# Performance work log

Hardware: AMD Instinct MI355X
Metric: run time of the kernel (lower is better)

## Reference

```python
import jax, jax.numpy as jnp
import numpy as np

B, D = 8192, 512
MARGIN, CR_BETA, NUM_CLASSES = 0.2, 0.1, 1000


def setup_inputs() -> dict:
    key = jax.random.key(0)
    k1, k2, k3, k4 = jax.random.split(key, 4)
    return {
        "img": jax.random.normal(k1, (B, D), jnp.float32),
        "txt": jax.random.normal(k2, (B, D), jnp.float32),
        "txt_cr": jax.random.normal(k3, (B, D), jnp.float32),
        "labels": jax.random.randint(k4, (B,), 0, NUM_CLASSES),
        "auto_margin_flag": 1,
        "margin": jnp.full((B,), MARGIN, jnp.float32),  # opt.margin repeated per row
        "cr_beta": CR_BETA,
    }


def _similarity(a, b):
    # row-normalize then full cosine-similarity matrix + matched (diagonal) sims
    an = a / (jnp.linalg.norm(a, axis=1, keepdims=True) + 1e-8)
    bn = b / (jnp.linalg.norm(b, axis=1, keepdims=True) + 1e-8)
    return an @ bn.T, jnp.sum(an * bn, axis=1)


def _dir_loss(sim, labels, margin, auto_flag):
    # semi-hard negative mining per anchor row, fully vectorized.
    # Deterministic stand-in for np.random.choice: first valid negative index.
    diag = jnp.diagonal(sim)                               # sim[idx, idx]
    neg_mask = labels[None, :] != labels[:, None]          # [B,B] negatives
    loss_mat = sim - diag[:, None] + margin[:, None]       # triplet margin term
    valid = neg_mask & (loss_mat > 0) & (loss_mat < margin[:, None])
    valid = jax.lax.stop_gradient(valid)                   # mining is detached (numpy in torch)
    has_valid = jnp.any(valid, axis=1)
    if auto_flag:
        row_ok = (margin >= 0.16) & has_valid
    else:
        row_ok = has_valid
    neg_idx = jnp.argmax(valid, axis=1)                    # first valid negative
    sim_an = jnp.take_along_axis(sim, neg_idx[:, None], axis=1)[:, 0]
    per_row = jax.nn.relu(margin - diag + sim_an)
    return jnp.sum(jnp.where(row_ok, per_row, 0.0))


def _cr_loss(img, txt, txt_cr, labels, auto_flag, margin, cr_beta):
    sim, sm = _similarity(img, txt)
    sim_cr, sm_cr = _similarity(img, txt_cr)
    if auto_flag:
        lam = jnp.abs(jax.lax.stop_gradient(sm_cr)) / jnp.abs(jax.lax.stop_gradient(sm))
        lam = jnp.minimum(lam, 1.0)                        # clamp lambda_cr to <= 1
        margin_cr = (lam + 1.0) * margin / 2.0
    else:
        margin_cr = margin / 2.0
    margin_cr = jax.lax.stop_gradient(margin_cr)
    base = _dir_loss(sim, labels, margin, auto_flag) + _dir_loss(sim.T, labels, margin, auto_flag)
    cr = _dir_loss(sim_cr, labels, margin_cr, auto_flag) + _dir_loss(sim_cr.T, labels, margin_cr, auto_flag)
    return base + cr_beta * cr


def reference(img, txt, txt_cr, labels, auto_margin_flag, margin, cr_beta):
    return _cr_loss(img, txt, txt_cr, labels, bool(auto_margin_flag), margin, cr_beta)
```

## Files before the change

kernel.cpp:

```cpp
#include <hip/hip_runtime.h>
#include <climits>

#define NB 8192
#define ND 512
#define NSPLIT 32
#define RSTART 64
#define RSPAN ((NB - RSTART + NSPLIT - 1) / NSPLIT)


__global__ __launch_bounds__(256) void stats_k(
        const float* __restrict__ img, const float* __restrict__ txt,
        const float* __restrict__ cr, const float* __restrict__ margin,
        const int* __restrict__ flagp,
        float* rnImg, float* rnTxt, float* rnCr,
        float* dgSim, float* dgCr, float* mgCr,
        int* negIdx, int* stragCnt, float* out) {
    int tid = threadIdx.x, bid = blockIdx.x;
    int g = bid * 256 + tid;
    if (g < 4 * NB) negIdx[g] = INT_MAX;
    if (bid == 0 && tid < 8) stragCnt[tid] = 0;
    if (bid == 0 && tid == 0) out[0] = 0.0f;

    int r = bid * 16 + (tid >> 4);
    int q = tid & 15;
    const float4* iv = (const float4*)(img + (size_t)r * ND);
    const float4* tv = (const float4*)(txt + (size_t)r * ND);
    const float4* cv = (const float4*)(cr  + (size_t)r * ND);
    float sii = 0, stt = 0, scc = 0, sit = 0, sic = 0;
    #pragma unroll
    for (int i = 0; i < 8; ++i) {
        int k = q + i * 16;
        float4 x = iv[k], y = tv[k], w = cv[k];
        sii += x.x*x.x + x.y*x.y + x.z*x.z + x.w*x.w;
        stt += y.x*y.x + y.y*y.y + y.z*y.z + y.w*y.w;
        scc += w.x*w.x + w.y*w.y + w.z*w.z + w.w*w.w;
        sit += x.x*y.x + x.y*y.y + x.z*y.z + x.w*y.w;
        sic += x.x*w.x + x.y*w.y + x.z*w.z + x.w*w.w;
    }
    #pragma unroll
    for (int off = 1; off < 16; off <<= 1) {
        sii += __shfl_xor(sii, off); stt += __shfl_xor(stt, off);
        scc += __shfl_xor(scc, off); sit += __shfl_xor(sit, off);
        sic += __shfl_xor(sic, off);
    }
    if (q == 0) {
        float rnI = 1.0f / (sqrtf(sii) + 1e-8f);
        float rnT = 1.0f / (sqrtf(stt) + 1e-8f);
        float rnC = 1.0f / (sqrtf(scc) + 1e-8f);
        float ds = sit * rnI * rnT;
        float dc = sic * rnI * rnC;
        float m  = margin[r];
        float mcr = flagp[0] ? (fminf(fabsf(dc) / fabsf(ds), 1.0f) + 1.0f) * m * 0.5f
                             : m * 0.5f;
        rnImg[r] = rnI; rnTxt[r] = rnT; rnCr[r] = rnC;
        dgSim[r] = ds;  dgCr[r]  = dc;  mgCr[r] = mcr;
    }
}

__device__ inline void pass_arrays(int z,
        const float* img, const float* txt, const float* cr,
        const float* rnImg, const float* rnTxt, const float* rnCr,
        const float* dgSim, const float* dgCr,
        const float* margin, const float* mgCr,
        const float*& A, const float*& B, const float*& rnA, const float*& rnB,
        const float*& dgA, const float*& mgA) {
    if (z == 0)      { A = img; B = txt; rnA = rnImg; rnB = rnTxt; dgA = dgSim; mgA = margin; }
    else if (z == 1) { A = txt; B = img; rnA = rnTxt; rnB = rnImg; dgA = dgSim; mgA = margin; }
    else if (z == 2) { A = img; B = cr;  rnA = rnImg; rnB = rnCr;  dgA = dgCr;  mgA = mgCr;   }
    else             { A = cr;  B = img; rnA = rnCr;  rnB = rnImg; dgA = dgCr;  mgA = mgCr;   }
}

__global__ __launch_bounds__(256) void band_k(
        const float* __restrict__ img, const float* __restrict__ txt,
        const float* __restrict__ cr, const int* __restrict__ labels,
        const int* __restrict__ flagp, const float* __restrict__ margin,
        const float* __restrict__ betap,
        const float* rnImg, const float* rnTxt, const float* rnCr,
        const float* dgSim, const float* dgCr, const float* mgCr,
        int* stragCnt, int* stragList, float* out) {
    __shared__ __align__(16) float As[16][64];
    __shared__ __align__(16) float Bs[16][64];
    __shared__ float aRn[64], aDg[64], aMg[64], colRn[64];
    __shared__ int   aLab[64], colLab[64], resIdx[64];
    __shared__ float blockAcc;

    const int tid = threadIdx.x, z = blockIdx.y, a0 = blockIdx.x * 64;
    const int flag = flagp[0];
    const float *A, *B, *rnA, *rnB, *dgA, *mgA;
    pass_arrays(z, img, txt, cr, rnImg, rnTxt, rnCr, dgSim, dgCr, margin, mgCr,
                A, B, rnA, rnB, dgA, mgA);

    if (tid < 64) {
        int a = a0 + tid;
        float mg = mgA[a];
        aRn[tid] = rnA[a]; aDg[tid] = dgA[a]; aMg[tid] = mg;
        aLab[tid] = labels[a];
        colRn[tid] = rnB[tid]; colLab[tid] = labels[tid];
        resIdx[tid] = (flag && mg < 0.16f) ? -1 : INT_MAX;
    }
    if (tid == 0) blockAcc = 0.0f;

    const int ty4  = (tid >> 4) * 4, tx4 = (tid & 15) * 4;
    const int lrow = tid >> 2,  lk4 = (tid & 3) * 4;

    float acc[4][4];
    #pragma unroll
    for (int i = 0; i < 4; ++i)
        #pragma unroll
        for (int j = 0; j < 4; ++j) acc[i][j] = 0.0f;

    float4 va = *(const float4*)(A + (size_t)(a0 + lrow) * ND + lk4);
    float4 vb = *(const float4*)(B + (size_t)lrow * ND + lk4);
    for (int kc = 0; kc < ND; kc += 16) {
        __syncthreads();
        As[lk4 + 0][lrow] = va.x; As[lk4 + 1][lrow] = va.y;
        As[lk4 + 2][lrow] = va.z; As[lk4 + 3][lrow] = va.w;
        Bs[lk4 + 0][lrow] = vb.x; Bs[lk4 + 1][lrow] = vb.y;
        Bs[lk4 + 2][lrow] = vb.z; Bs[lk4 + 3][lrow] = vb.w;
        if (kc + 16 < ND) {
            va = *(const float4*)(A + (size_t)(a0 + lrow) * ND + kc + 16 + lk4);
            vb = *(const float4*)(B + (size_t)lrow * ND + kc + 16 + lk4);
        }
        __syncthreads();
        #pragma unroll
        for (int k = 0; k < 16; ++k) {
            float4 av = *(const float4*)&As[k][ty4];
            float4 bv = *(const float4*)&Bs[k][tx4];
            float ar[4] = {av.x, av.y, av.z, av.w};
            float br[4] = {bv.x, bv.y, bv.z, bv.w};
            #pragma unroll
            for (int i = 0; i < 4; ++i)
                #pragma unroll
                for (int j = 0; j < 4; ++j)
                    acc[i][j] = fmaf(ar[i], br[j], acc[i][j]);
        }
    }
    __syncthreads();

    #pragma unroll
    for (int i = 0; i < 4; ++i) {
        int r = ty4 + i;
        float mgv = aMg[r];
        if (flag && mgv < 0.16f) continue;
        float dg = aDg[r], rna = aRn[r];
        int la = aLab[r];
        #pragma unroll
        for (int j = 0; j < 4; ++j) {
            int c = tx4 + j;
            if (colLab[c] == la) continue;
            float v  = acc[i][j] * rna * colRn[c];
            float lm = v - dg + mgv;
            if (lm > 0.0f && lm < mgv) atomicMin(&resIdx[r], c);
        }
    }
    __syncthreads();

    #pragma unroll
    for (int i = 0; i < 4; ++i) {
        int r = ty4 + i;
        int w = resIdx[r];
        if (w < 0 || w == INT_MAX) continue;
        int c = w - tx4;
        if (c < 0 || c > 3) continue;
        float v  = acc[i][c] * aRn[r] * colRn[w];
        float lm = v - aDg[r] + aMg[r];
        atomicAdd(&blockAcc, lm);
    }
    __syncthreads();

    if (tid < 64 && resIdx[tid] == INT_MAX) {
        int pos = atomicAdd(&stragCnt[z], 1);
        stragList[z * NB + pos] = a0 + tid;
    }
    if (tid == 0 && blockAcc != 0.0f) {
        float scale = (z >= 2) ? betap[0] : 1.0f;
        atomicAdd(out, blockAcc * scale);
    }
}

__device__ inline float dot8(const float4& a0, const float4& a1,
                             const float4& b0, const float4& b1) {
    return a0.x*b0.x + a0.y*b0.y + a0.z*b0.z + a0.w*b0.w
         + a1.x*b1.x + a1.y*b1.y + a1.z*b1.z + a1.w*b1.w;
}

__global__ __launch_bounds__(256) void strag_k(
        const float* __restrict__ img, const float* __restrict__ txt,
        const float* __restrict__ cr, const int* __restrict__ labels,
        const float* rnImg, const float* rnTxt, const float* rnCr,
        const float* dgSim, const float* dgCr,
        const float* __restrict__ margin, const float* mgCr,
        const int* stragCnt, const int* stragList, int* negIdx) {
    __shared__ float colDot[64];
    __shared__ int   cMin;
    __shared__ int   sharedG;
    const int tid = threadIdx.x;
    const int wv = tid >> 6, lane = tid & 63;

    const int s0c = stragCnt[0], s1c = stragCnt[1];
    const int s2c = stragCnt[2], s3c = stragCnt[3];
    const int ST = s0c + s1c + s2c + s3c;
    const int total = ST * NSPLIT;

    for (int it = blockIdx.x; it < total; it += gridDim.x) {
        int rg = it / ST;
        int sIdx = it - rg * ST;
        int z, s;
        if (sIdx < s0c)                 { z = 0; s = sIdx; }
        else if ((sIdx -= s0c) < s1c)   { z = 1; s = sIdx; }
        else if ((sIdx -= s1c) < s2c)   { z = 2; s = sIdx; }
        else                            { z = 3; s = sIdx - s2c; }
        const float *A, *B, *rnA, *rnB, *dgA, *mgA;
        pass_arrays(z, img, txt, cr, rnImg, rnTxt, rnCr, dgSim, dgCr,
                    margin, mgCr, A, B, rnA, rnB, dgA, mgA);
        int a = stragList[z * NB + s];
        int* gp = &negIdx[z * NB + a];
        const int start = RSTART + rg * RSPAN;
        const int rEnd = min(start + RSPAN, NB);

        __syncthreads();
        if (tid == 0) { cMin = INT_MAX; sharedG = atomicMin(gp, INT_MAX); }
        __syncthreads();
        int end = min(rEnd, sharedG);
        if (start >= end) continue;

        float rna = rnA[a], dgv = dgA[a], mgv = mgA[a];
        int la = labels[a];
        const float4* Av = (const float4*)(A + (size_t)a * ND);
        float4 ar0 = Av[lane], ar1 = Av[lane + 64];

        for (int j0 = start; j0 < end; j0 += 64) {
            #pragma unroll
            for (int g = 0; g < 2; ++g) {
                int cbase = j0 + wv * 16 + g * 8;
                float4 b0[8], b1[8];
                #pragma unroll
                for (int q = 0; q < 8; ++q) {
                    int col = cbase + q;
                    const float4* Bv = (col < end)
                        ? (const float4*)(B + (size_t)col * ND)
                        : (const float4*)B;
                    b0[q] = Bv[lane]; b1[q] = Bv[lane + 64];
                }
                float d[8];
                #pragma unroll
                for (int q = 0; q < 8; ++q) d[q] = dot8(ar0, ar1, b0[q], b1[q]);
                #pragma unroll
                for (int off = 1; off < 64; off <<= 1) {
                    #pragma unroll
                    for (int q = 0; q < 8; ++q) d[q] += __shfl_xor(d[q], off);
                }
                if (lane == 0) {
                    #pragma unroll
                    for (int q = 0; q < 8; ++q)
                        colDot[wv * 16 + g * 8 + q] = d[q];
                }
            }
            __syncthreads();
            if (tid < 64) {
                int col = j0 + tid;
                if (col < end && labels[col] != la) {
                    float lm = colDot[tid] * rna * rnB[col] - dgv + mgv;
                    if (lm > 0.0f && lm < mgv) atomicMin(&cMin, col);
                }
            } else if (tid == 64) {
                sharedG = atomicMin(gp, INT_MAX);
            }
            __syncthreads();
            int found = cMin;
            int gmin  = sharedG;
            if (found != INT_MAX) {
                if (tid == 0) atomicMin(gp, found);
                break;
            }
            if (gmin <= start) break;
            if (gmin < end) end = gmin;
        }
    }
}

__global__ __launch_bounds__(256) void final_k(
        const float* __restrict__ img, const float* __restrict__ txt,
        const float* __restrict__ cr,
        const float* rnImg, const float* rnTxt, const float* rnCr,
        const float* dgSim, const float* dgCr,
        const float* __restrict__ margin, const float* mgCr,
        const float* __restrict__ betap,
        const int* stragCnt, const int* stragList, const int* negIdx,
        float* out) {
    __shared__ float s4[4];
    const int tid = threadIdx.x, z = blockIdx.y;
    const float *A, *B, *rnA, *rnB, *dgA, *mgA;
    pass_arrays(z, img, txt, cr, rnImg, rnTxt, rnCr, dgSim, dgCr, margin, mgCr,
                A, B, rnA, rnB, dgA, mgA);
    int t = blockIdx.x * 256 + tid;
    float contrib = 0.0f;
    if (t < stragCnt[z]) {
        int a = stragList[z * NB + t];
        int idx = negIdx[z * NB + a];
        if (idx != INT_MAX) {
            const float4* Av = (const float4*)(A + (size_t)a   * ND);
            const float4* Bv = (const float4*)(B + (size_t)idx * ND);
            float d = 0.0f;
            #pragma unroll 8
            for (int i = 0; i < ND / 4; ++i) {
                float4 x = Av[i], y = Bv[i];
                d += x.x*y.x + x.y*y.y + x.z*y.z + x.w*y.w;
            }
            float lm = d * rnA[a] * rnB[idx] - dgA[a] + mgA[a];
            contrib = fmaxf(lm, 0.0f);
        }
    }
    #pragma unroll
    for (int off = 32; off; off >>= 1) contrib += __shfl_xor(contrib, off);
    if ((tid & 63) == 0) s4[tid >> 6] = contrib;
    __syncthreads();
    if (tid == 0) {
        float sum = s4[0] + s4[1] + s4[2] + s4[3];
        if (sum != 0.0f) atomicAdd(out, sum * ((z >= 2) ? betap[0] : 1.0f));
    }
}


__global__ __launch_bounds__(256) void zero_k(float* out, int n) {
    int g = blockIdx.x * 256 + threadIdx.x;
    if (g < n) out[g] = 0.0f;
}

template <int U>
__device__ void stragScan(const float* __restrict__ A, const float* __restrict__ B,
                          const int* __restrict__ labels, int a0, int u, int scol,
                          const int* sList, int g0,
                          const float* aRn, const float* aDg, const float* aMg,
                          const int* aLab, int* sMin8, int* doneMask,
                          float* blockAcc) {
    const int tid = threadIdx.x;
    float rn_s[U], dg_s[U], mg_s[U];
    int lab_s[U];
    const float4* Av[U];
    #pragma unroll
    for (int s = 0; s < U; ++s) {
        int slot = sList[g0 + (s < u ? s : 0)];
        rn_s[s] = aRn[slot]; dg_s[s] = aDg[slot]; mg_s[s] = aMg[slot];
        lab_s[s] = aLab[slot];
        Av[s] = (const float4*)(A + (size_t)(a0 + slot) * ND);
    }
    if (tid < U) sMin8[tid] = INT_MAX;
    if (tid == 0) *doneMask = 0;
    __syncthreads();
    for (int jb = scol; jb < NB; jb += 256) {
        int j = jb + tid;
        bool jv = (j < NB);
        int mask = *doneMask;
        float dot[U];
        #pragma unroll
        for (int s = 0; s < U; ++s) dot[s] = 0.0f;
        float ssq = 0.0f;
        if (jv) {
            const float4* Bv = (const float4*)(B + (size_t)j * ND);
            #pragma unroll 4
            for (int k4 = 0; k4 < ND / 4; ++k4) {
                float4 b = Bv[k4];
                ssq += b.x*b.x + b.y*b.y + b.z*b.z + b.w*b.w;
                #pragma unroll
                for (int s = 0; s < U; ++s) {
                    float4 a = Av[s][k4];
                    dot[s] += a.x*b.x + a.y*b.y + a.z*b.z + a.w*b.w;
                }
            }
        }
        float rnb = 1.0f / (sqrtf(ssq) + 1e-8f);
        int lj = jv ? labels[j] : -1;
        float lmv[U];
        #pragma unroll
        for (int s = 0; s < U; ++s) {
            lmv[s] = dot[s] * rn_s[s] * rnb - dg_s[s] + mg_s[s];
            if (jv && s < u && !((mask >> s) & 1) && lj != lab_s[s] &&
                lmv[s] > 0.0f && lmv[s] < mg_s[s])
                atomicMin(&sMin8[s], j);
        }
        __syncthreads();
        #pragma unroll
        for (int s = 0; s < U; ++s)
            if (jv && s < u && !((mask >> s) & 1) && sMin8[s] == j)
                atomicAdd(blockAcc, lmv[s]);
        __syncthreads();
        if (tid == 0) {
            int m2 = 0;
            for (int s = 0; s < u; ++s)
                if (sMin8[s] != INT_MAX) m2 |= (1 << s);
            *doneMask = m2;
        }
        __syncthreads();
        if (*doneMask == (1 << u) - 1) break;
    }
}

__global__ __launch_bounds__(256) void mine_k(const float* __restrict__ img,
                                              const float* __restrict__ txt,
                                              const float* __restrict__ cr,
                                              const int*   __restrict__ labels,
                                              const int*   __restrict__ flagp,
                                              const float* __restrict__ margin,
                                              const float* __restrict__ betap,
                                              float* __restrict__ out) {
    __shared__ __align__(16) float As[16][64];
    __shared__ __align__(16) float Bs[16][64];
    __shared__ float aRn[64], aDg[64], aMg[64];
    __shared__ int   aLab[64];
    __shared__ float colRn[64];
    __shared__ int   colLab[64];
    __shared__ int   resIdx[64], prevIdx[64];
    __shared__ int   cnt;
    __shared__ float blockAcc;
    __shared__ int   sList[64];
    __shared__ int   sCnt;
    __shared__ int   sMin8[8];
    __shared__ int   doneMask;

    const int tid  = threadIdx.x;
    const int z    = blockIdx.y;
    const int a0   = blockIdx.x * 64;
    const int flag = flagp[0];
    const float* A = (z == 1) ? txt : (z == 3) ? cr : img;
    const float* B = (z == 0) ? txt : (z == 2) ? cr : img;
    {
        int ar = tid >> 2, q = tid & 3;
        int a  = a0 + ar;
        const float4* iv = (const float4*)(img + (size_t)a * ND) + q * 32;
        const float4* tv = (const float4*)(txt + (size_t)a * ND) + q * 32;
        const float4* cv = (const float4*)(cr  + (size_t)a * ND) + q * 32;
        float sii = 0, stt = 0, scc = 0, sit = 0, sic = 0;
        #pragma unroll 4
        for (int i = 0; i < 32; ++i) {
            float4 x = iv[i], y = tv[i], w = cv[i];
            sii += x.x*x.x + x.y*x.y + x.z*x.z + x.w*x.w;
            stt += y.x*y.x + y.y*y.y + y.z*y.z + y.w*y.w;
            scc += w.x*w.x + w.y*w.y + w.z*w.z + w.w*w.w;
            sit += x.x*y.x + x.y*y.y + x.z*y.z + x.w*y.w;
            sic += x.x*w.x + x.y*w.y + x.z*w.z + x.w*w.w;
        }
        sii += __shfl_xor(sii, 1); sii += __shfl_xor(sii, 2);
        stt += __shfl_xor(stt, 1); stt += __shfl_xor(stt, 2);
        sit += __shfl_xor(sit, 1); sit += __shfl_xor(sit, 2);
        scc += __shfl_xor(scc, 1); scc += __shfl_xor(scc, 2);
        sic += __shfl_xor(sic, 1); sic += __shfl_xor(sic, 2);
        if (q == 0) {
            float rnI = 1.0f / (sqrtf(sii) + 1e-8f);
            float rnT = 1.0f / (sqrtf(stt) + 1e-8f);
            float ds  = sit * rnI * rnT;
            float m   = margin[a];
            float mg, rna, dgv;
            if (z >= 2) {
                float rnC = 1.0f / (sqrtf(scc) + 1e-8f);
                float dc  = sic * rnI * rnC;
                mg = flag ? (fminf(fabsf(dc) / fabsf(ds), 1.0f) + 1.0f) * m * 0.5f
                          : m * 0.5f;
                dgv = dc; rna = (z == 3) ? rnC : rnI;
            } else {
                mg = m; dgv = ds; rna = (z == 1) ? rnT : rnI;
            }
            aRn[ar] = rna; aDg[ar] = dgv; aMg[ar] = mg; aLab[ar] = labels[a];
            resIdx[ar] = (flag && mg < 0.16f) ? -1 : INT_MAX;
        }
        if (tid == 0) blockAcc = 0.0f;
    }
    __syncthreads();
    const int ty4  = (tid >> 4) * 4, tx4 = (tid & 15) * 4;
    const int lrow = tid >> 2,  lk4 = (tid & 3) * 4;
    int bandCols = 0, unresolved = 64;
    for (int jc = 0; jc < 2; ++jc) {
        int j0 = jc * 64;
        float acc[4][4];
        #pragma unroll
        for (int i = 0; i < 4; ++i)
            #pragma unroll
            for (int j = 0; j < 4; ++j) acc[i][j] = 0.0f;
        float bssq = 0.0f;
        for (int kc = 0; kc < ND; kc += 16) {
            __syncthreads();
            float4 va = *(const float4*)(A + (size_t)(a0 + lrow) * ND + kc + lk4);
            float4 vb = *(const float4*)(B + (size_t)(j0 + lrow) * ND + kc + lk4);
            As[lk4 + 0][lrow] = va.x; As[lk4 + 1][lrow] = va.y;
            As[lk4 + 2][lrow] = va.z; As[lk4 + 3][lrow] = va.w;
            Bs[lk4 + 0][lrow] = vb.x; Bs[lk4 + 1][lrow] = vb.y;
            Bs[lk4 + 2][lrow] = vb.z; Bs[lk4 + 3][lrow] = vb.w;
            bssq += vb.x*vb.x + vb.y*vb.y + vb.z*vb.z + vb.w*vb.w;
            __syncthreads();
            #pragma unroll
            for (int k = 0; k < 16; ++k) {
                float4 av = *(const float4*)&As[k][ty4];
                float4 bv = *(const float4*)&Bs[k][tx4];
                float ar[4] = {av.x, av.y, av.z, av.w};
                float br[4] = {bv.x, bv.y, bv.z, bv.w};
                #pragma unroll
                for (int i = 0; i < 4; ++i)
                    #pragma unroll
                    for (int j = 0; j < 4; ++j)
                        acc[i][j] = fmaf(ar[i], br[j], acc[i][j]);
            }
        }
        bssq += __shfl_xor(bssq, 1); bssq += __shfl_xor(bssq, 2);
        __syncthreads();
        if ((tid & 3) == 0) {
            colRn[lrow]  = 1.0f / (sqrtf(bssq) + 1e-8f);
            colLab[lrow] = labels[j0 + lrow];
        }
        if (tid < 64) prevIdx[tid] = resIdx[tid];
        __syncthreads();
        #pragma unroll
        for (int i = 0; i < 4; ++i) {
            int r = ty4 + i;
            if (prevIdx[r] != INT_MAX) continue;
            float dg = aDg[r], mgv = aMg[r], rna = aRn[r];
            int la = aLab[r];
            #pragma unroll
            for (int j = 0; j < 4; ++j) {
                int c = tx4 + j;
                if (colLab[c] == la) continue;
                float v  = acc[i][j] * rna * colRn[c];
                float lm = v - dg + mgv;
                if (lm > 0.0f && lm < mgv) atomicMin(&resIdx[r], j0 + c);
            }
        }
        __syncthreads();
        #pragma unroll
        for (int i = 0; i < 4; ++i) {
            int r = ty4 + i;
            if (prevIdx[r] != INT_MAX) continue;
            int w = resIdx[r];
            if (w == INT_MAX) continue;
            int c = w - j0 - tx4;
            if (c < 0 || c > 3) continue;
            float v  = acc[i][c] * aRn[r] * colRn[tx4 + c];
            float lm = v - aDg[r] + aMg[r];
            atomicAdd(&blockAcc, lm);
        }
        __syncthreads();
        if (tid == 0) cnt = 0;
        __syncthreads();
        if (tid < 64 && resIdx[tid] == INT_MAX) atomicAdd(&cnt, 1);
        __syncthreads();
        unresolved = cnt;
        bandCols = j0 + 64;
        __syncthreads();
        if (unresolved <= 8) break;
    }
    if (unresolved > 0) {
        if (tid == 0) sCnt = 0;
        __syncthreads();
        if (tid < 64 && resIdx[tid] == INT_MAX) {
            int pos = atomicAdd(&sCnt, 1);
            sList[pos] = tid;
        }
        __syncthreads();
        int total = sCnt;
        for (int g0 = 0; g0 < total; g0 += 8) {
            int u = min(8, total - g0);
            if (u == 1)      stragScan<1>(A, B, labels, a0, u, bandCols, sList, g0, aRn, aDg, aMg, aLab, sMin8, &doneMask, &blockAcc);
            else if (u == 2) stragScan<2>(A, B, labels, a0, u, bandCols, sList, g0, aRn, aDg, aMg, aLab, sMin8, &doneMask, &blockAcc);
            else if (u <= 4) stragScan<4>(A, B, labels, a0, u, bandCols, sList, g0, aRn, aDg, aMg, aLab, sMin8, &doneMask, &blockAcc);
            else             stragScan<8>(A, B, labels, a0, u, bandCols, sList, g0, aRn, aDg, aMg, aLab, sMin8, &doneMask, &blockAcc);
            __syncthreads();
        }
    }
    if (tid == 0 && blockAcc != 0.0f) {
        float scale = (z >= 2) ? betap[0] : 1.0f;
        atomicAdd(out, blockAcc * scale);
    }
}


extern "C" void kernel_launch(void* const* d_in, const int* in_sizes, int n_in,
                              void* d_out, int out_size, void* d_ws, size_t ws_size,
                              hipStream_t stream) {
    const float* img    = (const float*)d_in[0];
    const float* txt    = (const float*)d_in[1];
    const float* cr     = (const float*)d_in[2];
    const int*   labels = (const int*)  d_in[3];
    const int*   flagp  = (const int*)  d_in[4];
    const float* marg   = (const float*)d_in[5];
    const float* betap  = (const float*)d_in[6];
    float* out = (float*)d_out;
    (void)in_sizes; (void)n_in;

    const size_t REQ = (size_t)(6 * NB) * 4 + (size_t)(4 * NB) * 4 + 64 +
                       (size_t)(4 * NB) * 4;
    if (ws_size >= REQ) {
        float* wf = (float*)d_ws;
        float* rnImg = wf + 0 * NB;
        float* rnTxt = wf + 1 * NB;
        float* rnCr  = wf + 2 * NB;
        float* dgSim = wf + 3 * NB;
        float* dgCr  = wf + 4 * NB;
        float* mgCr  = wf + 5 * NB;
        int* negIdx    = (int*)(wf + 6 * NB);
        int* stragCnt  = negIdx + 4 * NB;
        int* stragList = stragCnt + 16;

        stats_k<<<dim3(NB / 16),      dim3(256), 0, stream>>>(
            img, txt, cr, marg, flagp,
            rnImg, rnTxt, rnCr, dgSim, dgCr, mgCr, negIdx, stragCnt, out);
        band_k <<<dim3(NB / 64, 4),   dim3(256), 0, stream>>>(
            img, txt, cr, labels, flagp, marg, betap,
            rnImg, rnTxt, rnCr, dgSim, dgCr, mgCr, stragCnt, stragList, out);
        strag_k<<<dim3(16384),        dim3(256), 0, stream>>>(
            img, txt, cr, labels, rnImg, rnTxt, rnCr, dgSim, dgCr, marg, mgCr,
            stragCnt, stragList, negIdx);
        final_k<<<dim3(NB / 256, 4),  dim3(256), 0, stream>>>(
            img, txt, cr, rnImg, rnTxt, rnCr, dgSim, dgCr, marg, mgCr, betap,
            stragCnt, stragList, negIdx, out);
    } else {
        zero_k<<<dim3((out_size + 255) / 256), dim3(256), 0, stream>>>(out, out_size);
        mine_k<<<dim3(NB / 64, 4), dim3(256), 0, stream>>>(img, txt, cr, labels,
                                                           flagp, marg, betap, out);
    }
}
```

Baseline: 220.0 us.

## Replace per-straggler shuffle-reduction search with tiled GEMM window and tail kernels

The old straggler search computed one dot product at a time per row, using cross-lane shuffle reductions and an early-exit scan over column ranges. It is replaced by two kernels that use 64x64 register-tiled SGEMM blocks staged through shared memory. The first kernel scans the first 16 column chunks for up to 256 stragglers per direction. The second gathers rows still unresolved and tiles them against every remaining 64-column chunk, using atomicMin to keep the first valid negative. This trades early termination for dense, reusable tile compute. It also caps survivors at 512 per direction, which silently drops rows if that cap is exceeded.

After: 229.1 us. 1.04x slower.

```diff
diff --git a/kernel.cpp b/kernel.cpp
--- a/kernel.cpp
+++ b/kernel.cpp
@@ -3,9 +3,10 @@
 
 #define NB 8192
 #define ND 512
-#define NSPLIT 32
-#define RSTART 64
-#define RSPAN ((NB - RSTART + NSPLIT - 1) / NSPLIT)
+
+#define WCHUNKS 16
+#define WMAXT 4
+#define TCHUNKS ((NB - 64) / 64)
 
 
 __global__ __launch_bounds__(256) void stats_k(
@@ -178,103 +179,195 @@
     }
 }
 
-__device__ inline float dot8(const float4& a0, const float4& a1,
-                             const float4& b0, const float4& b1) {
-    return a0.x*b0.x + a0.y*b0.y + a0.z*b0.z + a0.w*b0.w
-         + a1.x*b1.x + a1.y*b1.y + a1.z*b1.z + a1.w*b1.w;
-}
-
-__global__ __launch_bounds__(256) void strag_k(
+__global__ __launch_bounds__(256) void wina_k(
         const float* __restrict__ img, const float* __restrict__ txt,
         const float* __restrict__ cr, const int* __restrict__ labels,
+        const float* __restrict__ margin,
         const float* rnImg, const float* rnTxt, const float* rnCr,
-        const float* dgSim, const float* dgCr,
-        const float* __restrict__ margin, const float* mgCr,
+        const float* dgSim, const float* dgCr, const float* mgCr,
         const int* stragCnt, const int* stragList, int* negIdx) {
-    __shared__ float colDot[64];
-    __shared__ int   cMin;
-    __shared__ int   sharedG;
-    const int tid = threadIdx.x;
-    const int wv = tid >> 6, lane = tid & 63;
-
-    const int s0c = stragCnt[0], s1c = stragCnt[1];
-    const int s2c = stragCnt[2], s3c = stragCnt[3];
-    const int ST = s0c + s1c + s2c + s3c;
-    const int total = ST * NSPLIT;
-
-    for (int it = blockIdx.x; it < total; it += gridDim.x) {
-        int rg = it / ST;
-        int sIdx = it - rg * ST;
-        int z, s;
-        if (sIdx < s0c)                 { z = 0; s = sIdx; }
-        else if ((sIdx -= s0c) < s1c)   { z = 1; s = sIdx; }
-        else if ((sIdx -= s1c) < s2c)   { z = 2; s = sIdx; }
-        else                            { z = 3; s = sIdx - s2c; }
-        const float *A, *B, *rnA, *rnB, *dgA, *mgA;
-        pass_arrays(z, img, txt, cr, rnImg, rnTxt, rnCr, dgSim, dgCr,
-                    margin, mgCr, A, B, rnA, rnB, dgA, mgA);
+    __shared__ __align__(16) float As[16][64];
+    __shared__ __align__(16) float Bs[16][64];
+    __shared__ float aRn[64], aDg[64], aMg[64], colRn[64];
+    __shared__ int   aId[64], aRowS[64], aLab[64], colLab[64];
+
+    const int tid = threadIdx.x, z = blockIdx.y;
+    const int chunk = blockIdx.x & (WCHUNKS - 1);
+    const int t     = blockIdx.x / WCHUNKS;
+    const int cnt = stragCnt[z];
+    if (t * 64 >= cnt) return;
+    const int c0 = 64 + chunk * 64;
+
+    const float *A, *B, *rnA, *rnB, *dgA, *mgA;
+    pass_arrays(z, img, txt, cr, rnImg, rnTxt, rnCr, dgSim, dgCr, margin, mgCr,
+                A, B, rnA, rnB, dgA, mgA);
+
+    if (tid < 64) {
+        int s = t * 64 + tid;
+        int a = (s < cnt) ? stragList[z * NB + s] : -1;
+        int ar = (a >= 0) ? a : 0;
+        aId[tid] = a; aRowS[tid] = ar;
+        aRn[tid] = rnA[ar]; aDg[tid] = dgA[ar]; aMg[tid] = mgA[ar];
+        aLab[tid] = labels[ar];
+        colRn[tid] = rnB[c0 + tid]; colLab[tid] = labels[c0 + tid];
+    }
+    __syncthreads();
+
+    const int ty4  = (tid >> 4) * 4, tx4 = (tid & 15) * 4;
+    const int lrow = tid >> 2,  lk4 = (tid & 3) * 4;
+
+    float acc[4][4];
+    #pragma unroll
+    for (int i = 0; i < 4; ++i)
+        #pragma unroll
+        for (int j = 0; j < 4; ++j) acc[i][j] = 0.0f;
+
+    float4 va = *(const float4*)(A + (size_t)aRowS[lrow] * ND + lk4);
+    float4 vb = *(const float4*)(B + (size_t)(c0 + lrow) * ND + lk4);
+    for (int kc = 0; kc < ND; kc += 16) {
+        __syncthreads();
+        As[lk4 + 0][lrow] = va.x; As[lk4 + 1][lrow] = va.y;
+        As[lk4 + 2][lrow] = va.z; As[lk4 + 3][lrow] = va.w;
+        Bs[lk4 + 0][lrow] = vb.x; Bs[lk4 + 1][lrow] = vb.y;
+        Bs[lk4 + 2][lrow] = vb.z; Bs[lk4 + 3][lrow] = vb.w;
+        if (kc + 16 < ND) {
+            va = *(const float4*)(A + (size_t)aRowS[lrow] * ND + kc + 16 + lk4);
+            vb = *(const float4*)(B + (size_t)(c0 + lrow) * ND + kc + 16 + lk4);
+        }
+        __syncthreads();
+        #pragma unroll
+        for (int k = 0; k < 16; ++k) {
+            float4 av = *(const float4*)&As[k][ty4];
+            float4 bv = *(const float4*)&Bs[k][tx4];
+            float ar[4] = {av.x, av.y, av.z, av.w};
+            float br[4] = {bv.x, bv.y, bv.z, bv.w};
+            #pragma unroll
+            for (int i = 0; i < 4; ++i)
+                #pragma unroll
+                for (int j = 0; j < 4; ++j)
+                    acc[i][j] = fmaf(ar[i], br[j], acc[i][j]);
+        }
+    }
+    __syncthreads();
+
+    #pragma unroll
+    for (int i = 0; i < 4; ++i) {
+        int r = ty4 + i;
+        int a = aId[r];
+        if (a < 0) continue;
+        float dg = aDg[r], mgv = aMg[r], rna = aRn[r];
+        int la = aLab[r];
+        #pragma unroll
+        for (int j = 0; j < 4; ++j) {
+            int c = tx4 + j;
+            if (colLab[c] == la) continue;
+            float lm = acc[i][j] * rna * colRn[c] - dg + mgv;
+            if (lm > 0.0f && lm < mgv) atomicMin(&negIdx[z * NB + a], c0 + c);
+        }
+    }
+}
+
+__global__ __launch_bounds__(256) void tail_k(
+        const float* __restrict__ img, const float* __restrict__ txt,
+        const float* __restrict__ cr, const int* __restrict__ labels,
+        const float* __restrict__ margin,
+        const float* rnImg, const float* rnTxt, const float* rnCr,
+        const float* dgSim, const float* dgCr, const float* mgCr,
+        const int* stragCnt, const int* stragList, int* negIdx) {
+    __shared__ __align__(16) float As[16][64];
+    __shared__ __align__(16) float Bs[16][64];
+    __shared__ float aRn[64], aDg[64], aMg[64], colRn[64];
+    __shared__ int   aId[64], aRowS[64], aLab[64], colLab[64];
+    __shared__ int   sSurv[512];
+    __shared__ int   sNa;
+
+    const int tid = threadIdx.x, z = blockIdx.y;
+    const int c0 = 64 + blockIdx.x * 64;
+    const int cnt = stragCnt[z];
+    if (cnt == 0) return;
+
+    const float *A, *B, *rnA, *rnB, *dgA, *mgA;
+    pass_arrays(z, img, txt, cr, rnImg, rnTxt, rnCr, dgSim, dgCr, margin, mgCr,
+                A, B, rnA, rnB, dgA, mgA);
+
+    if (tid == 0) sNa = 0;
+    __syncthreads();
+    for (int s = tid; s < cnt; s += 256) {
         int a = stragList[z * NB + s];
-        int* gp = &negIdx[z * NB + a];
-        const int start = RSTART + rg * RSPAN;
-        const int rEnd = min(start + RSPAN, NB);
-
-        __syncthreads();
-        if (tid == 0) { cMin = INT_MAX; sharedG = atomicMin(gp, INT_MAX); }
-        __syncthreads();
-        int end = min(rEnd, sharedG);
-        if (start >= end) continue;
-
-        float rna = rnA[a], dgv = dgA[a], mgv = mgA[a];
-        int la = labels[a];
-        const float4* Av = (const float4*)(A + (size_t)a * ND);
-        float4 ar0 = Av[lane], ar1 = Av[lane + 64];
-
-        for (int j0 = start; j0 < end; j0 += 64) {
+        if (negIdx[z * NB + a] == INT_MAX) {
+            int p = atomicAdd(&sNa, 1);
+            if (p < 512) sSurv[p] = a;
+        }
+    }
+    __syncthreads();
+    const int na = min(sNa, 512);
+    if (na == 0) return;
+
+    if (tid < 64) { colRn[tid] = rnB[c0 + tid]; colLab[tid] = labels[c0 + tid]; }
+
+    const int ty4  = (tid >> 4) * 4, tx4 = (tid & 15) * 4;
+    const int lrow = tid >> 2,  lk4 = (tid & 3) * 4;
+
+    for (int s0 = 0; s0 < na; s0 += 64) {
+        __syncthreads();
+        if (tid < 64) {
+            int s = s0 + tid;
+            int a = (s < na) ? sSurv[s] : -1;
+            int ar = (a >= 0) ? a : 0;
+            aId[tid] = a; aRowS[tid] = ar;
+            aRn[tid] = rnA[ar]; aDg[tid] = dgA[ar]; aMg[tid] = mgA[ar];
+            aLab[tid] = labels[ar];
+        }
+        __syncthreads();
+
+        float acc[4][4];
+        #pragma unroll
+        for (int i = 0; i < 4; ++i)
             #pragma unroll
-            for (int g = 0; g < 2; ++g) {
-                int cbase = j0 + wv * 16 + g * 8;
-                float4 b0[8], b1[8];
-                #pragma unroll
-                for (int q = 0; q < 8; ++q) {
-                    int col = cbase + q;
-                    const float4* Bv = (col < end)
-                        ? (const float4*)(B + (size_t)col * ND)
-                        : (const float4*)B;
-                    b0[q] = Bv[lane]; b1[q] = Bv[lane + 64];
-                }
-                float d[8];
-                #pragma unroll
-                for (int q = 0; q < 8; ++q) d[q] = dot8(ar0, ar1, b0[q], b1[q]);
-                #pragma unroll
-                for (int off = 1; off < 64; off <<= 1) {
-                    #pragma unroll
-                    for (int q = 0; q < 8; ++q) d[q] += __shfl_xor(d[q], off);
-                }
-                if (lane == 0) {
-                    #pragma unroll
-                    for (int q = 0; q < 8; ++q)
-                        colDot[wv * 16 + g * 8 + q] = d[q];
-                }
+            for (int j = 0; j < 4; ++j) acc[i][j] = 0.0f;
+
+        float4 va = *(const float4*)(A + (size_t)aRowS[lrow] * ND + lk4);
+        float4 vb = *(const float4*)(B + (size_t)(c0 + lrow) * ND + lk4);
+        for (int kc = 0; kc < ND; kc += 16) {
+            __syncthreads();
+            As[lk4 + 0][lrow] = va.x; As[lk4 + 1][lrow] = va.y;
+            As[lk4 + 2][lrow] = va.z; As[lk4 + 3][lrow] = va.w;
+            Bs[lk4 + 0][lrow] = vb.x; Bs[lk4 + 1][lrow] = vb.y;
+            Bs[lk4 + 2][lrow] = vb.z; Bs[lk4 + 3][lrow] = vb.w;
+            if (kc + 16 < ND) {
+                va = *(const float4*)(A + (size_t)aRowS[lrow] * ND + kc + 16 + lk4);
+                vb = *(const float4*)(B + (size_t)(c0 + lrow) * ND + kc + 16 + lk4);
             }
             __syncthreads();
-            if (tid < 64) {
-                int col = j0 + tid;
-                if (col < end && labels[col] != la) {
-                    float lm = colDot[tid] * rna * rnB[col] - dgv + mgv;
-                    if (lm > 0.0f && lm < mgv) atomicMin(&cMin, col);
-                }
-            } else if (tid == 64) {
-                sharedG = atomicMin(gp, INT_MAX);
+            #pragma unroll
+            for (int k = 0; k < 16; ++k) {
+                float4 av = *(const float4*)&As[k][ty4];
+                float4 bv = *(const float4*)&Bs[k][tx4];
+                float ar[4] = {av.x, av.y, av.z, av.w};
+                float br[4] = {bv.x, bv.y, bv.z, bv.w};
+                #pragma unroll
+                for (int i = 0; i < 4; ++i)
+                    #pragma unroll
+                    for (int j = 0; j < 4; ++j)
+                        acc[i][j] = fmaf(ar[i], br[j], acc[i][j]);
             }
-            __syncthreads();
-            int found = cMin;
-            int gmin  = sharedG;
-            if (found != INT_MAX) {
-                if (tid == 0) atomicMin(gp, found);
-                break;
+        }
+        __syncthreads();
+
+        #pragma unroll
+        for (int i = 0; i < 4; ++i) {
+            int r = ty4 + i;
+            int a = aId[r];
+            if (a < 0) continue;
+            float dg = aDg[r], mgv = aMg[r], rna = aRn[r];
+            int la = aLab[r];
+            #pragma unroll
+            for (int j = 0; j < 4; ++j) {
+                int c = tx4 + j;
+                if (colLab[c] == la) continue;
+                float lm = acc[i][j] * rna * colRn[c] - dg + mgv;
+                if (lm > 0.0f && lm < mgv) atomicMin(&negIdx[z * NB + a], c0 + c);
             }
-            if (gmin <= start) break;
-            if (gmin < end) end = gmin;
         }
     }
 }
@@ -598,16 +691,21 @@
         int* stragCnt  = negIdx + 4 * NB;
         int* stragList = stragCnt + 16;
 
-        stats_k<<<dim3(NB / 16),      dim3(256), 0, stream>>>(
+        stats_k<<<dim3(NB / 16),              dim3(256), 0, stream>>>(
             img, txt, cr, marg, flagp,
             rnImg, rnTxt, rnCr, dgSim, dgCr, mgCr, negIdx, stragCnt, out);
-        band_k <<<dim3(NB / 64, 4),   dim3(256), 0, stream>>>(
+        band_k <<<dim3(NB / 64, 4),           dim3(256), 0, stream>>>(
             img, txt, cr, labels, flagp, marg, betap,
             rnImg, rnTxt, rnCr, dgSim, dgCr, mgCr, stragCnt, stragList, out);
-        strag_k<<<dim3(16384),        dim3(256), 0, stream>>>(
-            img, txt, cr, labels, rnImg, rnTxt, rnCr, dgSim, dgCr, marg, mgCr,
+        wina_k <<<dim3(WCHUNKS * WMAXT, 4),   dim3(256), 0, stream>>>(
+            img, txt, cr, labels, marg,
+            rnImg, rnTxt, rnCr, dgSim, dgCr, mgCr,
             stragCnt, stragList, negIdx);
-        final_k<<<dim3(NB / 256, 4),  dim3(256), 0, stream>>>(
+        tail_k <<<dim3(TCHUNKS, 4),           dim3(256), 0, stream>>>(
+            img, txt, cr, labels, marg,
+            rnImg, rnTxt, rnCr, dgSim, dgCr, mgCr,
+            stragCnt, stragList, negIdx);
+        final_k<<<dim3(NB / 256, 4),          dim3(256), 0, stream>>>(
             img, txt, cr, rnImg, rnTxt, rnCr, dgSim, dgCr, marg, mgCr, betap,
             stragCnt, stragList, negIdx, out);
     } else {
```
